# Kernel tuning notes

Hardware: AMD Instinct MI355X
Metric: run time of the kernel (lower is better)

## Reference

```python
import jax, jax.numpy as jnp
import numpy as np

D_MODEL = 768
D_STATE = 16
D_CONV = 4
D_INNER = 2 * D_MODEL          # expand=2
DT_RANK = (D_MODEL + 15) // 16 # ceil(d_model/16), official Mamba default
N_LAYERS = 4
N_VOCAB = 2048
LN_EPS = 1e-5


def _silu(x):
    return x * jax.nn.sigmoid(x)


def _layer_norm(x, g, b):
    mu = jnp.mean(x, axis=-1, keepdims=True)
    var = jnp.mean(jnp.square(x - mu), axis=-1, keepdims=True)
    return (x - mu) * jax.lax.rsqrt(var + LN_EPS) * g + b


def _mamba_block(x, W_in, conv_w, conv_b, W_x, W_dt, b_dt, A_log, D_skip, W_out):
    # x: [B, L, D_MODEL]
    Bsz, L, _ = x.shape
    xz = x @ W_in                              # [B, L, 2*D_INNER]
    xc, z = jnp.split(xz, 2, axis=-1)
    # causal depthwise conv over time
    xt = xc.transpose(0, 2, 1)                 # [B, D_INNER, L]
    kern = conv_w[:, None, :]                  # [D_INNER, 1, D_CONV]
    xt = jax.lax.conv_general_dilated(
        xt, kern, window_strides=(1,), padding=[(D_CONV - 1, 0)],
        dimension_numbers=('NCH', 'OIH', 'NCH'), feature_group_count=D_INNER)
    u = _silu(xt.transpose(0, 2, 1) + conv_b)  # [B, L, D_INNER]
    # input-dependent SSM params
    dbl = u @ W_x                              # [B, L, DT_RANK + 2*D_STATE]
    dt, Bm, Cm = jnp.split(dbl, [DT_RANK, DT_RANK + D_STATE], axis=-1)
    delta = jax.nn.softplus(dt @ W_dt + b_dt)  # [B, L, D_INNER]
    A = -jnp.exp(A_log)                        # [D_INNER, D_STATE], negative

    def step(h, inp):
        d_t, B_t, C_t, u_t = inp               # [B,Di],[B,N],[B,N],[B,Di]
        dA = jnp.exp(d_t[..., None] * A)       # [B, D_INNER, D_STATE]
        dBu = (d_t * u_t)[..., None] * B_t[:, None, :]
        h = dA * h + dBu
        y = jnp.einsum('bdn,bn->bd', h, C_t)
        return h, y

    h0 = jnp.zeros((Bsz, D_INNER, D_STATE), x.dtype)
    _, ys = jax.lax.scan(step, h0, (delta.transpose(1, 0, 2),
                                    Bm.transpose(1, 0, 2),
                                    Cm.transpose(1, 0, 2),
                                    u.transpose(1, 0, 2)))
    y = ys.transpose(1, 0, 2) + u * D_skip     # skip connection D*u
    y = y * _silu(z)                           # gating
    return y @ W_out                           # [B, L, D_MODEL]


def setup_inputs() -> dict:
    key = jax.random.key(0)
    ks = jax.random.split(key, 12)
    B, L = 2, 2048
    s = 0.02
    tokens = jax.random.randint(ks[0], (B, L), 0, N_VOCAB)
    emb = jax.random.normal(ks[1], (N_VOCAB + 1, D_MODEL), jnp.float32) * s
    emb = emb.at[N_VOCAB].set(0.0)  # padding_idx row
    in_proj_w = jax.random.normal(ks[2], (N_LAYERS, D_MODEL, 2 * D_INNER), jnp.float32) * s
    conv_w = jax.random.normal(ks[3], (N_LAYERS, D_INNER, D_CONV), jnp.float32) * s
    conv_b = jnp.zeros((N_LAYERS, D_INNER), jnp.float32)
    x_proj_w = jax.random.normal(ks[4], (N_LAYERS, D_INNER, DT_RANK + 2 * D_STATE), jnp.float32) * s
    dt_proj_w = jax.random.normal(ks[5], (N_LAYERS, DT_RANK, D_INNER), jnp.float32) * s
    # dt bias so softplus(bias) lands in [1e-3, 0.1] (standard Mamba dt init)
    dt = jnp.exp(jax.random.uniform(ks[6], (N_LAYERS, D_INNER)) * (np.log(0.1) - np.log(1e-3)) + np.log(1e-3))
    dt_proj_b = dt + jnp.log(-jnp.expm1(-dt))  # inverse softplus
    A_log = jnp.log(jnp.tile(jnp.arange(1, D_STATE + 1, dtype=jnp.float32), (N_LAYERS, D_INNER, 1)))
    skip_D = jnp.ones((N_LAYERS, D_INNER), jnp.float32)
    out_proj_w = jax.random.normal(ks[7], (N_LAYERS, D_INNER, D_MODEL), jnp.float32) * s
    ln_g = jnp.ones((N_LAYERS, D_MODEL), jnp.float32)
    ln_b = jnp.zeros((N_LAYERS, D_MODEL), jnp.float32)
    head_w = jax.random.normal(ks[8], (D_MODEL, N_VOCAB), jnp.float32) * s
    head_b = jnp.zeros((N_VOCAB,), jnp.float32)
    return dict(tokens=tokens, emb=emb, in_proj_w=in_proj_w, conv_w=conv_w,
                conv_b=conv_b, x_proj_w=x_proj_w, dt_proj_w=dt_proj_w,
                dt_proj_b=dt_proj_b, A_log=A_log, skip_D=skip_D,
                out_proj_w=out_proj_w, ln_g=ln_g, ln_b=ln_b,
                head_w=head_w, head_b=head_b)


def reference(tokens, emb, in_proj_w, conv_w, conv_b, x_proj_w, dt_proj_w,
              dt_proj_b, A_log, skip_D, out_proj_w, ln_g, ln_b, head_w, head_b):
    x = emb[tokens]                            # [B, L, D_MODEL]
    for i in range(N_LAYERS):                  # post-norm residual (prenorm=False)
        z = _mamba_block(x, in_proj_w[i], conv_w[i], conv_b[i], x_proj_w[i],
                         dt_proj_w[i], dt_proj_b[i], A_log[i], skip_D[i],
                         out_proj_w[i])
        x = x + z                              # dropout=0 (identity)
        x = _layer_norm(x, ln_g[i], ln_b[i])
    return x @ head_w + head_b                 # [B, L, N_VOCAB]
```

## Files before the change

kernel.cpp:

```cpp
#include <hip/hip_runtime.h>
#include <hip/hip_bf16.h>
#include <math.h>

#define BSZ 2
#define SEQ 2048
#define DM 768
#define DI 1536
#define DS 16
#define DTR 48
#define NL 4
#define NV 2048
#define LNEPS 1e-5f
#define MROWS (BSZ * SEQ)
#define CCH 32
#define TCH 64
#define KSPLIT 12

typedef __hip_bfloat16 bf16;
typedef unsigned short u16t;
typedef __attribute__((ext_vector_type(8))) short short8;
typedef __attribute__((ext_vector_type(4))) float f32x4;

__device__ __forceinline__ bool probe_bf16(const void* p) {
    const u16t* q = (const u16t*)p;
    return q[0] == 0x3F80 && q[1] == 0x3F80;
}
__device__ __forceinline__ float ldany(const void* p, size_t i, bool bf) {
    if (bf) {
        unsigned u = (unsigned)(((const u16t*)p)[i]) << 16;
        return __uint_as_float(u);
    }
    return ((const float*)p)[i];
}
__device__ __forceinline__ float ldb(const bf16* p, size_t i) { return __bfloat162float(p[i]); }
__device__ __forceinline__ void stb(bf16* p, size_t i, float v) { p[i] = __float2bfloat16(v); }
__device__ __forceinline__ float bits2f(u16t b) { return __uint_as_float((unsigned)b << 16); }
__device__ __forceinline__ u16t f2bbits(float f) {
    unsigned x = __float_as_uint(f);
    return (u16t)((x + 0x7fffu + ((x >> 16) & 1u)) >> 16);
}
__device__ __forceinline__ u16t ld_bfbits(const void* p, size_t i, bool bf) {
    if (bf) return ((const u16t*)p)[i];
    return f2bbits(((const float*)p)[i]);
}
__device__ __forceinline__ float softplus_fast(float x) {
    if (x > 20.f) return x;
    return 0.69314718056f * __log2f(1.f + __expf(x));
}
__device__ __forceinline__ float siluf(float x) { return x / (1.f + __expf(-x)); }

__global__ __launch_bounds__(256) void embed_kernel(const int* __restrict__ tokens,
                                                    const void* __restrict__ emb,
                                                    bf16* __restrict__ X,
                                                    const void* __restrict__ probe) {
    bool bf = probe_bf16(probe);
    int idx = blockIdx.x * 256 + threadIdx.x;
    if (idx >= MROWS * DM) return;
    int c = idx % DM;
    int bl = idx / DM;
    stb(X, idx, ldany(emb, (size_t)tokens[bl] * DM + c, bf));
}

__global__ __launch_bounds__(256) void transpose_w(const void* __restrict__ W, size_t woff,
                                                   bf16* __restrict__ WT, int K, int N,
                                                   const void* __restrict__ probe) {
    bool bf = probe_bf16(probe);
    __shared__ u16t T[64][65];
    const int n0 = blockIdx.x * 64, k0 = blockIdx.y * 64;
    const int tid = threadIdx.x;
#pragma unroll
    for (int it = 0; it < 16; ++it) {
        int j = tid + 256 * it;
        int r = j >> 6, c = j & 63;
        T[r][c] = ld_bfbits(W, woff + (size_t)(k0 + r) * N + n0 + c, bf);
    }
    __syncthreads();
#pragma unroll
    for (int it = 0; it < 2; ++it) {
        int j = tid + 256 * it;
        int c = j >> 3, r8 = (j & 7) * 8;
        u16t tmp[8];
#pragma unroll
        for (int e = 0; e < 8; ++e) tmp[e] = T[r8 + e][c];
        *reinterpret_cast<uint4*>(WT + (size_t)(n0 + c) * K + k0 + r8) =
            *reinterpret_cast<const uint4*>(tmp);
    }
}

template <int MODE>
__global__ __launch_bounds__(256) void gemm_bt(const bf16* __restrict__ A, int lda,
                                               const bf16* __restrict__ BT,
                                               const void* __restrict__ bias, size_t bioff,
                                               bf16* __restrict__ Cb, void* __restrict__ Cout,
                                               int N, int K,
                                               const void* __restrict__ probe) {
    __shared__ u16t Alds[128 * 40];
    __shared__ u16t Blds[128 * 40];
    const int tid = threadIdx.x;
    const int lane = tid & 63, w = tid >> 6;
    const int wr = w >> 1, wc = w & 1;
    const int l15 = lane & 15, l4 = lane >> 4;
    const int row0 = blockIdx.y * 128, col0 = blockIdx.x * 128;
    f32x4 acc[4][4];
#pragma unroll
    for (int i = 0; i < 4; ++i)
#pragma unroll
        for (int j = 0; j < 4; ++j) acc[i][j] = (f32x4){0.f, 0.f, 0.f, 0.f};

    for (int k0 = 0; k0 < K; k0 += 32) {
#pragma unroll
        for (int j = 0; j < 2; ++j) {
            int i = tid + 256 * j;
            int r = i >> 2, c8 = (i & 3) * 8;
            uint4 va = *reinterpret_cast<const uint4*>(A + (size_t)(row0 + r) * lda + k0 + c8);
            *reinterpret_cast<uint4*>(&Alds[r * 40 + c8]) = va;
            uint4 vb = *reinterpret_cast<const uint4*>(BT + (size_t)(col0 + r) * K + k0 + c8);
            *reinterpret_cast<uint4*>(&Blds[r * 40 + c8]) = vb;
        }
        __syncthreads();
        short8 af[4], bfr[4];
#pragma unroll
        for (int fi = 0; fi < 4; ++fi)
            af[fi] = *reinterpret_cast<const short8*>(&Alds[(wr * 64 + fi * 16 + l15) * 40 + l4 * 8]);
#pragma unroll
        for (int fj = 0; fj < 4; ++fj)
            bfr[fj] = *reinterpret_cast<const short8*>(&Blds[(wc * 64 + fj * 16 + l15) * 40 + l4 * 8]);
#pragma unroll
        for (int fi = 0; fi < 4; ++fi)
#pragma unroll
            for (int fj = 0; fj < 4; ++fj)
                acc[fi][fj] = __builtin_amdgcn_mfma_f32_16x16x32_bf16(af[fi], bfr[fj],
                                                                      acc[fi][fj], 0, 0, 0);
        __syncthreads();
    }
    bool bf = probe_bf16(probe);
#pragma unroll
    for (int fi = 0; fi < 4; ++fi) {
        int row = row0 + wr * 64 + fi * 16 + l4 * 4;
#pragma unroll
        for (int fj = 0; fj < 4; ++fj) {
            int col = col0 + wc * 64 + fj * 16 + l15;
#pragma unroll
            for (int r = 0; r < 4; ++r) {
                float v = acc[fi][fj][r];
                size_t off = (size_t)(row + r) * N + col;
                if (MODE == 2) {
                    float o = v + ldany(bias, bioff + col, bf);
                    if (bf) stb((bf16*)Cout, off, o);
                    else ((float*)Cout)[off] = o;
                } else {
                    stb(Cb, off, v);
                }
            }
        }
    }
}

__global__ __launch_bounds__(256) void xproj_mfma(const bf16* __restrict__ A,
                                                  const void* __restrict__ B, size_t boff,
                                                  float* __restrict__ XPART,
                                                  const void* __restrict__ probe) {
    bool bf = probe_bf16(probe);
    __shared__ u16t Alds[128 * 40];
    __shared__ u16t Blds[80 * 40];
    const int tid = threadIdx.x;
    const int lane = tid & 63, w = tid >> 6;
    const int l15 = lane & 15, l4 = lane >> 4;
    const int z = blockIdx.x, row0 = blockIdx.y * 128;
    f32x4 acc[2][5];
#pragma unroll
    for (int i = 0; i < 2; ++i)
#pragma unroll
        for (int j = 0; j < 5; ++j) acc[i][j] = (f32x4){0.f, 0.f, 0.f, 0.f};

    for (int ks = 0; ks < 4; ++ks) {
        int kbase = z * 128 + ks * 32;
#pragma unroll
        for (int j = 0; j < 2; ++j) {
            int i = tid + 256 * j;
            int r = i >> 2, c8 = (i & 3) * 8;
            uint4 v = *reinterpret_cast<const uint4*>(A + (size_t)(row0 + r) * DI + kbase + c8);
            *reinterpret_cast<uint4*>(&Alds[r * 40 + c8]) = v;
        }
        for (int i = tid; i < 320; i += 256) {
            int kk = i / 10, c8 = (i % 10) * 8;
            u16t tmp[8];
            if (bf) {
                uint4 v = *reinterpret_cast<const uint4*>((const u16t*)B + boff +
                                                          (size_t)(kbase + kk) * 80 + c8);
                const u16t* s = (const u16t*)&v;
#pragma unroll
                for (int e = 0; e < 8; ++e) tmp[e] = s[e];
            } else {
                const float* Bf = (const float*)B + boff + (size_t)(kbase + kk) * 80 + c8;
#pragma unroll
                for (int e = 0; e < 8; ++e) tmp[e] = f2bbits(Bf[e]);
            }
#pragma unroll
            for (int e = 0; e < 8; ++e) Blds[(c8 + e) * 40 + kk] = tmp[e];
        }
        __syncthreads();
        short8 af[2], bfr[5];
#pragma unroll
        for (int fi = 0; fi < 2; ++fi)
            af[fi] = *reinterpret_cast<const short8*>(&Alds[(w * 32 + fi * 16 + l15) * 40 + l4 * 8]);
#pragma unroll
        for (int fj = 0; fj < 5; ++fj)
            bfr[fj] = *reinterpret_cast<const short8*>(&Blds[(fj * 16 + l15) * 40 + l4 * 8]);
#pragma unroll
        for (int fi = 0; fi < 2; ++fi)
#pragma unroll
            for (int fj = 0; fj < 5; ++fj)
                acc[fi][fj] = __builtin_amdgcn_mfma_f32_16x16x32_bf16(af[fi], bfr[fj],
                                                                      acc[fi][fj], 0, 0, 0);
        __syncthreads();
    }
#pragma unroll
    for (int fi = 0; fi < 2; ++fi) {
        int row = row0 + w * 32 + fi * 16 + l4 * 4;
#pragma unroll
        for (int fj = 0; fj < 5; ++fj) {
            int col = fj * 16 + l15;
#pragma unroll
            for (int r = 0; r < 4; ++r)
                XPART[((size_t)z * MROWS + row + r) * 80 + col] = acc[fi][fj][r];
        }
    }
}

__global__ __launch_bounds__(256) void xreduce_kernel(const float* __restrict__ XPART,
                                                      bf16* __restrict__ DBL) {
    int idx = blockIdx.x * 256 + threadIdx.x;
    float s = 0.f;
#pragma unroll
    for (int z = 0; z < KSPLIT; ++z) s += XPART[(size_t)z * MROWS * 80 + idx];
    stb(DBL, idx, s);
}

__global__ __launch_bounds__(256) void dtproj_valu(const bf16* __restrict__ DBL,
                                                   const void* __restrict__ Wdt, size_t woff,
                                                   const void* __restrict__ bias, size_t bioff,
                                                   bf16* __restrict__ DELTA,
                                                   const void* __restrict__ probe) {
    bool bf = probe_bf16(probe);
    __shared__ float Wlds[48 * 132];
    __shared__ float Dlds[64 * 49];
    const int tid = threadIdx.x;
    const int tx = tid & 15, ty = tid >> 4;
    const int col0 = blockIdx.x * 128, rows0 = blockIdx.y * 64;
#pragma unroll
    for (int it = 0; it < 24; ++it) {
        int j = tid + 256 * it;
        int k = j >> 7, c = j & 127;
        Wlds[k * 132 + c] = ldany(Wdt, woff + (size_t)k * DI + col0 + c, bf);
    }
#pragma unroll
    for (int it = 0; it < 12; ++it) {
        int j = tid + 256 * it;
        int r = j / 48, k = j % 48;
        Dlds[r * 49 + k] = ldb(DBL, (size_t)(rows0 + r) * 80 + k);
    }
    __syncthreads();
    float acc[4][8] = {};
#pragma unroll 4
    for (int k = 0; k < 48; ++k) {
        float4 w0 = *reinterpret_cast<const float4*>(&Wlds[k * 132 + tx * 8]);
        float4 w1 = *reinterpret_cast<const float4*>(&Wlds[k * 132 + tx * 8 + 4]);
        float wv[8] = {w0.x, w0.y, w0.z, w0.w, w1.x, w1.y, w1.z, w1.w};
#pragma unroll
        for (int r = 0; r < 4; ++r) {
            float d = Dlds[(ty * 4 + r) * 49 + k];
#pragma unroll
            for (int e = 0; e < 8; ++e) acc[r][e] += d * wv[e];
        }
    }
    float bj[8];
#pragma unroll
    for (int e = 0; e < 8; ++e) bj[e] = ldany(bias, bioff + col0 + tx * 8 + e, bf);
#pragma unroll
    for (int r = 0; r < 4; ++r) {
        u16t tmp[8];
#pragma unroll
        for (int e = 0; e < 8; ++e) tmp[e] = f2bbits(softplus_fast(acc[r][e] + bj[e]));
        *reinterpret_cast<uint4*>(DELTA + (size_t)(rows0 + ty * 4 + r) * DI + col0 + tx * 8) =
            *reinterpret_cast<const uint4*>(tmp);
    }
}

__global__ __launch_bounds__(256) void conv_silu_v8(const bf16* __restrict__ XZ,
                                                    const void* __restrict__ cw, size_t cwoff,
                                                    const void* __restrict__ cb, size_t cboff,
                                                    bf16* __restrict__ U,
                                                    const void* __restrict__ probe) {
    bool bf = probe_bf16(probe);
    int idx = blockIdx.x * 256 + threadIdx.x;
    int dp = idx % (DI / 8);
    int bl = idx / (DI / 8);
    int d0 = dp * 8;
    int l = bl % SEQ;
    int b = bl / SEQ;
    float s[8];
#pragma unroll
    for (int e = 0; e < 8; ++e) s[e] = ldany(cb, cboff + d0 + e, bf);
#pragma unroll
    for (int k = 0; k < 4; ++k) {
        int lt = l - 3 + k;
        if (lt < 0) continue;
        uint4 v = *reinterpret_cast<const uint4*>((const u16t*)XZ +
                                                  (size_t)(b * SEQ + lt) * 2 * DI + d0);
        const u16t* xv = (const u16t*)&v;
#pragma unroll
        for (int e = 0; e < 8; ++e)
            s[e] += ldany(cw, cwoff + (size_t)(d0 + e) * 4 + k, bf) * bits2f(xv[e]);
    }
    u16t out[8];
#pragma unroll
    for (int e = 0; e < 8; ++e) out[e] = f2bbits(siluf(s[e]));
    *reinterpret_cast<uint4*>((u16t*)U + (size_t)bl * DI + d0) =
        *reinterpret_cast<const uint4*>(out);
}

__global__ __launch_bounds__(256) void scan_phase1(const bf16* __restrict__ DELTA,
                                                   const bf16* __restrict__ U,
                                                   const bf16* __restrict__ DBL,
                                                   const void* __restrict__ A_log, size_t aoff,
                                                   float* __restrict__ P, float* __restrict__ Q,
                                                   const void* __restrict__ probe) {
    bool bf = probe_bf16(probe);
    int blk = blockIdx.x;
    int dt = blk % (2 * DI / 256);
    int t2 = blk / (2 * DI / 256);
    int c = t2 % CCH;
    int b = t2 / CCH;
    int g = dt * 256 + threadIdx.x;
    int d = g >> 1, s = g & 1;
    float An[8], h[8], q[8];
#pragma unroll
    for (int n = 0; n < 8; ++n) {
        An[n] = -__expf(ldany(A_log, aoff + (size_t)d * DS + s * 8 + n, bf));
        h[n] = 0.f;
        q[n] = 1.f;
    }
    int t0 = c * TCH;
    const bf16* dpp = DELTA + (size_t)(b * SEQ + t0) * DI + d;
    const bf16* up = U + (size_t)(b * SEQ + t0) * DI + d;
    const u16t* bcp = (const u16t*)DBL + (size_t)(b * SEQ + t0) * 80 + DTR + s * 8;
    float del = ldb(dpp, 0), u = ldb(up, 0);
    uint4 b0 = *reinterpret_cast<const uint4*>(bcp);
    for (int t = 0; t < TCH; ++t) {
        float delc = del, uc = u;
        uint4 c0 = b0;
        if (t + 1 < TCH) {
            dpp += DI; up += DI; bcp += 80;
            del = ldb(dpp, 0);
            u = ldb(up, 0);
            b0 = *reinterpret_cast<const uint4*>(bcp);
        }
        float du = delc * uc;
        const u16t* bs = (const u16t*)&c0;
#pragma unroll
        for (int n = 0; n < 8; ++n) {
            float Bn = bits2f(bs[n]);
            float dA = __expf(delc * An[n]);
            h[n] = dA * h[n] + du * Bn;
            q[n] *= dA;
        }
    }
    size_t o = ((((size_t)b * CCH + c) * DI) + d) * 16 + s * 8;
    *reinterpret_cast<float4*>(&P[o]) = (float4){h[0], h[1], h[2], h[3]};
    *reinterpret_cast<float4*>(&P[o + 4]) = (float4){h[4], h[5], h[6], h[7]};
    *reinterpret_cast<float4*>(&Q[o]) = (float4){q[0], q[1], q[2], q[3]};
    *reinterpret_cast<float4*>(&Q[o + 4]) = (float4){q[4], q[5], q[6], q[7]};
}

__global__ __launch_bounds__(256) void scan_phase2(const float* __restrict__ P,
                                                   const float* __restrict__ Q,
                                                   float* __restrict__ H0) {
    int g = blockIdx.x * 256 + threadIdx.x;
    int n = g & 15;
    int rest = g >> 4;
    int d = rest % DI;
    int b = rest / DI;
    float S = 0.f;
    for (int c = 0; c < CCH; ++c) {
        size_t idx = ((((size_t)b * CCH + c) * DI) + d) * 16 + n;
        H0[idx] = S;
        S = Q[idx] * S + P[idx];
    }
}

__global__ __launch_bounds__(256) void scan_phase3(const bf16* __restrict__ DELTA,
                                                   bf16* __restrict__ U,
                                                   const bf16* __restrict__ DBL,
                                                   const bf16* __restrict__ XZ,
                                                   const float* __restrict__ H0,
                                                   const void* __restrict__ A_log, size_t aoff,
                                                   const void* __restrict__ Dskip, size_t doff,
                                                   const void* __restrict__ probe) {
    bool bf = probe_bf16(probe);
    int blk = blockIdx.x;
    int dt = blk % (2 * DI / 256);
    int t2 = blk / (2 * DI / 256);
    int c = t2 % CCH;
    int b = t2 / CCH;
    int g = dt * 256 + threadIdx.x;
    int d = g >> 1, s = g & 1;
    float An[8], h[8];
    size_t ho = ((((size_t)b * CCH + c) * DI) + d) * 16 + s * 8;
#pragma unroll
    for (int n = 0; n < 8; ++n) {
        An[n] = -__expf(ldany(A_log, aoff + (size_t)d * DS + s * 8 + n, bf));
        h[n] = H0[ho + n];
    }
    float Dk = ldany(Dskip, doff + d, bf);
    int t0 = c * TCH;
    const bf16* dpp = DELTA + (size_t)(b * SEQ + t0) * DI + d;
    const bf16* zp = XZ + (size_t)(b * SEQ + t0) * 2 * DI + DI + d;
    const u16t* bcp = (const u16t*)DBL + (size_t)(b * SEQ + t0) * 80 + DTR + s * 8;
    const bf16* up = U + (size_t)(b * SEQ + t0) * DI + d;
    float del = ldb(dpp, 0), u = ldb(up, 0), z = ldb(zp, 0);
    uint4 b0 = *reinterpret_cast<const uint4*>(bcp);
    uint4 b1 = *reinterpret_cast<const uint4*>(bcp + 16);
    for (int t = 0; t < TCH; ++t) {
        float delc = del, uc = u, zc = z;
        uint4 c0 = b0, c1 = b1;
        if (t + 1 < TCH) {
            dpp += DI; up += DI; zp += 2 * DI; bcp += 80;
            del = ldb(dpp, 0);
            u = ldb(up, 0);
            z = ldb(zp, 0);
            b0 = *reinterpret_cast<const uint4*>(bcp);
            b1 = *reinterpret_cast<const uint4*>(bcp + 16);
        }
        float du = delc * uc;
        const u16t* bs = (const u16t*)&c0;
        const u16t* cs = (const u16t*)&c1;
        float y = 0.f;
#pragma unroll
        for (int n = 0; n < 8; ++n) {
            float Bn = bits2f(bs[n]);
            float Cn = bits2f(cs[n]);
            float dA = __expf(delc * An[n]);
            h[n] = dA * h[n] + du * Bn;
            y += h[n] * Cn;
        }
        y += __shfl_xor(y, 1);
        if (s == 0)
            stb(U, (size_t)(b * SEQ + t0 + t) * DI + d, (y + uc * Dk) * siluf(zc));
    }
}

__global__ __launch_bounds__(192) void add_ln_v4(const bf16* __restrict__ O,
                                                 bf16* __restrict__ X,
                                                 const void* __restrict__ g, size_t goff,
                                                 const void* __restrict__ be, size_t beoff,
                                                 const void* __restrict__ probe) {
    bool bf = probe_bf16(probe);
    int row = blockIdx.x;
    int t = threadIdx.x;
    int c0 = t * 4;
    __shared__ float wred[6];
    uint2 xv = *reinterpret_cast<const uint2*>((const u16t*)X + (size_t)row * DM + c0);
    uint2 ov = *reinterpret_cast<const uint2*>((const u16t*)O + (size_t)row * DM + c0);
    const u16t* xs = (const u16t*)&xv;
    const u16t* os = (const u16t*)&ov;
    float v[4];
    float part = 0.f;
#pragma unroll
    for (int e = 0; e < 4; ++e) {
        v[e] = bits2f(xs[e]) + bits2f(os[e]);
        part += v[e];
    }
#pragma unroll
    for (int o = 32; o > 0; o >>= 1) part += __shfl_down(part, o, 64);
    int wid = t >> 6, lane = t & 63;
    if (lane == 0) wred[wid] = part;
    __syncthreads();
    float mean = (wred[0] + wred[1] + wred[2]) * (1.f / DM);
    float p2 = 0.f;
#pragma unroll
    for (int e = 0; e < 4; ++e) {
        float dv = v[e] - mean;
        p2 += dv * dv;
    }
#pragma unroll
    for (int o = 32; o > 0; o >>= 1) p2 += __shfl_down(p2, o, 64);
    if (lane == 0) wred[3 + wid] = p2;
    __syncthreads();
    float rs = rsqrtf((wred[3] + wred[4] + wred[5]) * (1.f / DM) + LNEPS);
    u16t out[4];
#pragma unroll
    for (int e = 0; e < 4; ++e)
        out[e] = f2bbits((v[e] - mean) * rs * ldany(g, goff + c0 + e, bf) +
                         ldany(be, beoff + c0 + e, bf));
    *reinterpret_cast<uint2*>((u16t*)X + (size_t)row * DM + c0) =
        *reinterpret_cast<const uint2*>(out);
}

extern "C" void kernel_launch(void* const* d_in, const int* in_sizes, int n_in,
                              void* d_out, int out_size, void* d_ws, size_t ws_size,
                              hipStream_t stream) {
    const int* tokens = (const int*)d_in[0];
    const void* emb = d_in[1];
    const void* in_proj_w = d_in[2];
    const void* conv_w = d_in[3];
    const void* conv_b = d_in[4];
    const void* x_proj_w = d_in[5];
    const void* dt_proj_w = d_in[6];
    const void* dt_proj_b = d_in[7];
    const void* A_log = d_in[8];
    const void* skip_D = d_in[9];
    const void* out_proj_w = d_in[10];
    const void* ln_g = d_in[11];
    const void* ln_b = d_in[12];
    const void* head_w = d_in[13];
    const void* head_b = d_in[14];
    const void* probe = ln_g;

    bf16* X = (bf16*)d_ws;
    bf16* XZ = X + (size_t)MROWS * DM;
    bf16* Ub = XZ + (size_t)MROWS * 2 * DI;
    bf16* DBL = Ub + (size_t)MROWS * DI;
    bf16* DELTA = DBL + (size_t)MROWS * 80;
    bf16* O = DELTA;
    float* P = (float*)(DELTA + (size_t)MROWS * DI);
    float* Q = P + (size_t)BSZ * CCH * DI * 16;
    float* H0 = Q + (size_t)BSZ * CCH * DI * 16;
    float* XPART = P;
    bf16* WT1 = (bf16*)(H0 + (size_t)BSZ * CCH * DI * 16);
    bf16* WT2 = WT1 + (size_t)(2 * DI) * DM;

    embed_kernel<<<(MROWS * DM + 255) / 256, 256, 0, stream>>>(tokens, emb, X, probe);

    for (int i = 0; i < NL; ++i) {
        transpose_w<<<dim3(2 * DI / 64, DM / 64), 256, 0, stream>>>(
            in_proj_w, (size_t)i * DM * 2 * DI, WT1, DM, 2 * DI, probe);
        transpose_w<<<dim3(DM / 64, DI / 64), 256, 0, stream>>>(
            out_proj_w, (size_t)i * DI * DM, WT2, DI, DM, probe);
        gemm_bt<0><<<dim3(2 * DI / 128, MROWS / 128), 256, 0, stream>>>(
            X, DM, WT1, nullptr, 0, XZ, nullptr, 2 * DI, DM, probe);
        conv_silu_v8<<<(MROWS * DI / 8) / 256, 256, 0, stream>>>(
            XZ, conv_w, (size_t)i * DI * 4, conv_b, (size_t)i * DI, Ub, probe);
        xproj_mfma<<<dim3(KSPLIT, MROWS / 128), 256, 0, stream>>>(
            Ub, x_proj_w, (size_t)i * DI * 80, XPART, probe);
        xreduce_kernel<<<(MROWS * 80) / 256, 256, 0, stream>>>(XPART, DBL);
        dtproj_valu<<<dim3(DI / 128, MROWS / 64), 256, 0, stream>>>(
            DBL, dt_proj_w, (size_t)i * DTR * DI, dt_proj_b, (size_t)i * DI, DELTA, probe);
        scan_phase1<<<BSZ * CCH * (2 * DI / 256), 256, 0, stream>>>(
            DELTA, Ub, DBL, A_log, (size_t)i * DI * DS, P, Q, probe);
        scan_phase2<<<(BSZ * DI * 16) / 256, 256, 0, stream>>>(P, Q, H0);
        scan_phase3<<<BSZ * CCH * (2 * DI / 256), 256, 0, stream>>>(
            DELTA, Ub, DBL, XZ, H0, A_log, (size_t)i * DI * DS, skip_D, (size_t)i * DI, probe);
        gemm_bt<0><<<dim3(DM / 128, MROWS / 128), 256, 0, stream>>>(
            Ub, DI, WT2, nullptr, 0, O, nullptr, DM, DI, probe);
        add_ln_v4<<<MROWS, 192, 0, stream>>>(O, X, ln_g, (size_t)i * DM, ln_b,
                                             (size_t)i * DM, probe);
    }
    transpose_w<<<dim3(NV / 64, DM / 64), 256, 0, stream>>>(head_w, 0, WT1, DM, NV, probe);
    gemm_bt<2><<<dim3(NV / 128, MROWS / 128), 256, 0, stream>>>(
        X, DM, WT1, head_b, 0, nullptr, d_out, NV, DM, probe);
}
```

Before: 1.352 ms.

## Use direct global-to-LDS loads with swizzle in GEMM, vectorize conv weights, widen scan parallelism

The GEMM now loads 64-wide K tiles straight from global memory into LDS with global_load_lds and an XOR swizzle, replacing register-staged copies into a padded layout, and runs two MFMA k-substeps per barrier pair. The conv kernel loads its weights and bias as vectors once per thread instead of making per-element typed loads. The scan phases split each channel's 16 states across 4 threads instead of 2, doubling the thread count and adding one more shuffle reduction. The aim is to cut GEMM staging overhead and raise occupancy for the latency-bound scan, at the cost of more redundant delta/u loads in the scan.

```diff
diff --git a/kernel.cpp b/kernel.cpp
--- a/kernel.cpp
+++ b/kernel.cpp
@@ -94,8 +94,8 @@
                                                bf16* __restrict__ Cb, void* __restrict__ Cout,
                                                int N, int K,
                                                const void* __restrict__ probe) {
-    __shared__ u16t Alds[128 * 40];
-    __shared__ u16t Blds[128 * 40];
+    __shared__ u16t Alds[128 * 64];
+    __shared__ u16t Blds[128 * 64];
     const int tid = threadIdx.x;
     const int lane = tid & 63, w = tid >> 6;
     const int wr = w >> 1, wc = w & 1;
@@ -107,30 +107,46 @@
 #pragma unroll
         for (int j = 0; j < 4; ++j) acc[i][j] = (f32x4){0.f, 0.f, 0.f, 0.f};
 
-    for (int k0 = 0; k0 < K; k0 += 32) {
-#pragma unroll
-        for (int j = 0; j < 2; ++j) {
-            int i = tid + 256 * j;
-            int r = i >> 2, c8 = (i & 3) * 8;
-            uint4 va = *reinterpret_cast<const uint4*>(A + (size_t)(row0 + r) * lda + k0 + c8);
-            *reinterpret_cast<uint4*>(&Alds[r * 40 + c8]) = va;
-            uint4 vb = *reinterpret_cast<const uint4*>(BT + (size_t)(col0 + r) * K + k0 + c8);
-            *reinterpret_cast<uint4*>(&Blds[r * 40 + c8]) = vb;
+    const int wavebase = tid & ~63;
+
+    for (int kt = 0; kt < K; kt += 64) {
+#pragma unroll
+        for (int it = 0; it < 4; ++it) {
+            int q = it * 256 + tid;
+            int r = q >> 3, j = q & 7;
+            int gk = (j ^ (r & 7)) * 8;
+            __builtin_amdgcn_global_load_lds(
+                (const __attribute__((address_space(1))) void*)(A + (size_t)(row0 + r) * lda + kt + gk),
+                (__attribute__((address_space(3))) void*)(Alds + (size_t)(it * 256 + wavebase) * 8),
+                16, 0, 0);
+            __builtin_amdgcn_global_load_lds(
+                (const __attribute__((address_space(1))) void*)(BT + (size_t)(col0 + r) * K + kt + gk),
+                (__attribute__((address_space(3))) void*)(Blds + (size_t)(it * 256 + wavebase) * 8),
+                16, 0, 0);
         }
         __syncthreads();
-        short8 af[4], bfr[4];
-#pragma unroll
-        for (int fi = 0; fi < 4; ++fi)
-            af[fi] = *reinterpret_cast<const short8*>(&Alds[(wr * 64 + fi * 16 + l15) * 40 + l4 * 8]);
-#pragma unroll
-        for (int fj = 0; fj < 4; ++fj)
-            bfr[fj] = *reinterpret_cast<const short8*>(&Blds[(wc * 64 + fj * 16 + l15) * 40 + l4 * 8]);
-#pragma unroll
-        for (int fi = 0; fi < 4; ++fi)
-#pragma unroll
-            for (int fj = 0; fj < 4; ++fj)
-                acc[fi][fj] = __builtin_amdgcn_mfma_f32_16x16x32_bf16(af[fi], bfr[fj],
-                                                                      acc[fi][fj], 0, 0, 0);
+#pragma unroll
+        for (int ks = 0; ks < 2; ++ks) {
+            short8 af[4], bfr[4];
+#pragma unroll
+            for (int fi = 0; fi < 4; ++fi) {
+                int R = wr * 64 + fi * 16 + l15;
+                int slot = (ks * 4 + l4) ^ (R & 7);
+                af[fi] = *reinterpret_cast<const short8*>(&Alds[R * 64 + slot * 8]);
+            }
+#pragma unroll
+            for (int fj = 0; fj < 4; ++fj) {
+                int R = wc * 64 + fj * 16 + l15;
+                int slot = (ks * 4 + l4) ^ (R & 7);
+                bfr[fj] = *reinterpret_cast<const short8*>(&Blds[R * 64 + slot * 8]);
+            }
+#pragma unroll
+            for (int fi = 0; fi < 4; ++fi)
+#pragma unroll
+                for (int fj = 0; fj < 4; ++fj)
+                    acc[fi][fj] = __builtin_amdgcn_mfma_f32_16x16x32_bf16(af[fi], bfr[fj],
+                                                                          acc[fi][fj], 0, 0, 0);
+        }
         __syncthreads();
     }
     bool bf = probe_bf16(probe);
@@ -299,9 +315,37 @@
     int d0 = dp * 8;
     int l = bl % SEQ;
     int b = bl / SEQ;
+    float wv[4][8];
     float s[8];
-#pragma unroll
-    for (int e = 0; e < 8; ++e) s[e] = ldany(cb, cboff + d0 + e, bf);
+    if (bf) {
+        const u16t* W = (const u16t*)cw + cwoff + (size_t)d0 * 4;
+#pragma unroll
+        for (int qd = 0; qd < 4; ++qd) {
+            uint4 wq = *reinterpret_cast<const uint4*>(W + qd * 8);
+            const u16t* ws = (const u16t*)&wq;
+#pragma unroll
+            for (int mm = 0; mm < 8; ++mm) {
+                int m = qd * 8 + mm;
+                wv[m & 3][m >> 2] = bits2f(ws[mm]);
+            }
+        }
+        uint4 bq = *reinterpret_cast<const uint4*>((const u16t*)cb + cboff + d0);
+        const u16t* bsp = (const u16t*)&bq;
+#pragma unroll
+        for (int e = 0; e < 8; ++e) s[e] = bits2f(bsp[e]);
+    } else {
+        const float* W = (const float*)cw + cwoff + (size_t)d0 * 4;
+#pragma unroll
+        for (int e = 0; e < 8; ++e) {
+            float4 f = *reinterpret_cast<const float4*>(W + e * 4);
+            wv[0][e] = f.x; wv[1][e] = f.y; wv[2][e] = f.z; wv[3][e] = f.w;
+        }
+        const float* Bp = (const float*)cb + cboff + d0;
+        float4 f0 = *reinterpret_cast<const float4*>(Bp);
+        float4 f1 = *reinterpret_cast<const float4*>(Bp + 4);
+        s[0] = f0.x; s[1] = f0.y; s[2] = f0.z; s[3] = f0.w;
+        s[4] = f1.x; s[5] = f1.y; s[6] = f1.z; s[7] = f1.w;
+    }
 #pragma unroll
     for (int k = 0; k < 4; ++k) {
         int lt = l - 3 + k;
@@ -310,8 +354,7 @@
                                                   (size_t)(b * SEQ + lt) * 2 * DI + d0);
         const u16t* xv = (const u16t*)&v;
 #pragma unroll
-        for (int e = 0; e < 8; ++e)
-            s[e] += ldany(cw, cwoff + (size_t)(d0 + e) * 4 + k, bf) * bits2f(xv[e]);
+        for (int e = 0; e < 8; ++e) s[e] += wv[k][e] * bits2f(xv[e]);
     }
     u16t out[8];
 #pragma unroll
@@ -328,49 +371,47 @@
                                                    const void* __restrict__ probe) {
     bool bf = probe_bf16(probe);
     int blk = blockIdx.x;
-    int dt = blk % (2 * DI / 256);
-    int t2 = blk / (2 * DI / 256);
+    int dt = blk % (4 * DI / 256);
+    int t2 = blk / (4 * DI / 256);
     int c = t2 % CCH;
     int b = t2 / CCH;
     int g = dt * 256 + threadIdx.x;
-    int d = g >> 1, s = g & 1;
-    float An[8], h[8], q[8];
-#pragma unroll
-    for (int n = 0; n < 8; ++n) {
-        An[n] = -__expf(ldany(A_log, aoff + (size_t)d * DS + s * 8 + n, bf));
+    int d = g >> 2, s = g & 3;
+    float An[4], h[4], q[4];
+#pragma unroll
+    for (int n = 0; n < 4; ++n) {
+        An[n] = -__expf(ldany(A_log, aoff + (size_t)d * DS + s * 4 + n, bf));
         h[n] = 0.f;
         q[n] = 1.f;
     }
     int t0 = c * TCH;
     const bf16* dpp = DELTA + (size_t)(b * SEQ + t0) * DI + d;
     const bf16* up = U + (size_t)(b * SEQ + t0) * DI + d;
-    const u16t* bcp = (const u16t*)DBL + (size_t)(b * SEQ + t0) * 80 + DTR + s * 8;
+    const u16t* bcp = (const u16t*)DBL + (size_t)(b * SEQ + t0) * 80 + DTR + s * 4;
     float del = ldb(dpp, 0), u = ldb(up, 0);
-    uint4 b0 = *reinterpret_cast<const uint4*>(bcp);
+    uint2 b0 = *reinterpret_cast<const uint2*>(bcp);
     for (int t = 0; t < TCH; ++t) {
         float delc = del, uc = u;
-        uint4 c0 = b0;
+        uint2 c0 = b0;
         if (t + 1 < TCH) {
             dpp += DI; up += DI; bcp += 80;
             del = ldb(dpp, 0);
             u = ldb(up, 0);
-            b0 = *reinterpret_cast<const uint4*>(bcp);
+            b0 = *reinterpret_cast<const uint2*>(bcp);
         }
         float du = delc * uc;
         const u16t* bs = (const u16t*)&c0;
 #pragma unroll
-        for (int n = 0; n < 8; ++n) {
+        for (int n = 0; n < 4; ++n) {
             float Bn = bits2f(bs[n]);
             float dA = __expf(delc * An[n]);
             h[n] = dA * h[n] + du * Bn;
             q[n] *= dA;
         }
     }
-    size_t o = ((((size_t)b * CCH + c) * DI) + d) * 16 + s * 8;
+    size_t o = ((((size_t)b * CCH + c) * DI) + d) * 16 + s * 4;
     *reinterpret_cast<float4*>(&P[o]) = (float4){h[0], h[1], h[2], h[3]};
-    *reinterpret_cast<float4*>(&P[o + 4]) = (float4){h[4], h[5], h[6], h[7]};
     *reinterpret_cast<float4*>(&Q[o]) = (float4){q[0], q[1], q[2], q[3]};
-    *reinterpret_cast<float4*>(&Q[o + 4]) = (float4){q[4], q[5], q[6], q[7]};
 }
 
 __global__ __launch_bounds__(256) void scan_phase2(const float* __restrict__ P,
@@ -399,45 +440,45 @@
                                                    const void* __restrict__ probe) {
     bool bf = probe_bf16(probe);
     int blk = blockIdx.x;
-    int dt = blk % (2 * DI / 256);
-    int t2 = blk / (2 * DI / 256);
+    int dt = blk % (4 * DI / 256);
+    int t2 = blk / (4 * DI / 256);
     int c = t2 % CCH;
     int b = t2 / CCH;
     int g = dt * 256 + threadIdx.x;
-    int d = g >> 1, s = g & 1;
-    float An[8], h[8];
-    size_t ho = ((((size_t)b * CCH + c) * DI) + d) * 16 + s * 8;
-#pragma unroll
-    for (int n = 0; n < 8; ++n) {
-        An[n] = -__expf(ldany(A_log, aoff + (size_t)d * DS + s * 8 + n, bf));
+    int d = g >> 2, s = g & 3;
+    float An[4], h[4];
+    size_t ho = ((((size_t)b * CCH + c) * DI) + d) * 16 + s * 4;
+#pragma unroll
+    for (int n = 0; n < 4; ++n) {
+        An[n] = -__expf(ldany(A_log, aoff + (size_t)d * DS + s * 4 + n, bf));
         h[n] = H0[ho + n];
     }
     float Dk = ldany(Dskip, doff + d, bf);
     int t0 = c * TCH;
     const bf16* dpp = DELTA + (size_t)(b * SEQ + t0) * DI + d;
     const bf16* zp = XZ + (size_t)(b * SEQ + t0) * 2 * DI + DI + d;
-    const u16t* bcp = (const u16t*)DBL + (size_t)(b * SEQ + t0) * 80 + DTR + s * 8;
+    const u16t* bcp = (const u16t*)DBL + (size_t)(b * SEQ + t0) * 80 + DTR + s * 4;
     const bf16* up = U + (size_t)(b * SEQ + t0) * DI + d;
     float del = ldb(dpp, 0), u = ldb(up, 0), z = ldb(zp, 0);
-    uint4 b0 = *reinterpret_cast<const uint4*>(bcp);
-    uint4 b1 = *reinterpret_cast<const uint4*>(bcp + 16);
+    uint2 b0 = *reinterpret_cast<const uint2*>(bcp);
+    uint2 b1 = *reinterpret_cast<const uint2*>(bcp + 16);
     for (int t = 0; t < TCH; ++t) {
         float delc = del, uc = u, zc = z;
-        uint4 c0 = b0, c1 = b1;
+        uint2 c0 = b0, c1 = b1;
         if (t + 1 < TCH) {
             dpp += DI; up += DI; zp += 2 * DI; bcp += 80;
             del = ldb(dpp, 0);
             u = ldb(up, 0);
             z = ldb(zp, 0);
-            b0 = *reinterpret_cast<const uint4*>(bcp);
-            b1 = *reinterpret_cast<const uint4*>(bcp + 16);
+            b0 = *reinterpret_cast<const uint2*>(bcp);
+            b1 = *reinterpret_cast<const uint2*>(bcp + 16);
         }
         float du = delc * uc;
         const u16t* bs = (const u16t*)&c0;
         const u16t* cs = (const u16t*)&c1;
         float y = 0.f;
 #pragma unroll
-        for (int n = 0; n < 8; ++n) {
+        for (int n = 0; n < 4; ++n) {
             float Bn = bits2f(bs[n]);
             float Cn = bits2f(cs[n]);
             float dA = __expf(delc * An[n]);
@@ -445,6 +486,7 @@
             y += h[n] * Cn;
         }
         y += __shfl_xor(y, 1);
+        y += __shfl_xor(y, 2);
         if (s == 0)
             stb(U, (size_t)(b * SEQ + t0 + t) * DI + d, (y + uc * Dk) * siluf(zc));
     }
@@ -546,10 +588,10 @@
         xreduce_kernel<<<(MROWS * 80) / 256, 256, 0, stream>>>(XPART, DBL);
         dtproj_valu<<<dim3(DI / 128, MROWS / 64), 256, 0, stream>>>(
             DBL, dt_proj_w, (size_t)i * DTR * DI, dt_proj_b, (size_t)i * DI, DELTA, probe);
-        scan_phase1<<<BSZ * CCH * (2 * DI / 256), 256, 0, stream>>>(
+        scan_phase1<<<BSZ * CCH * (4 * DI / 256), 256, 0, stream>>>(
             DELTA, Ub, DBL, A_log, (size_t)i * DI * DS, P, Q, probe);
         scan_phase2<<<(BSZ * DI * 16) / 256, 256, 0, stream>>>(P, Q, H0);
-        scan_phase3<<<BSZ * CCH * (2 * DI / 256), 256, 0, stream>>>(
+        scan_phase3<<<BSZ * CCH * (4 * DI / 256), 256, 0, stream>>>(
             DELTA, Ub, DBL, XZ, H0, A_log, (size_t)i * DI * DS, skip_D, (size_t)i * DI, probe);
         gemm_bt<0><<<dim3(DM / 128, MROWS / 128), 256, 0, stream>>>(
             Ub, DI, WT2, nullptr, 0, O, nullptr, DM, DI, probe);
```

After: 1.153 ms. 1.17x faster.
